# Kernel optimization log

Hardware: AMD Instinct MI355X
Metric: run time of the kernel (lower is better)

Reference implementation:

```python
import jax, jax.numpy as jnp
import numpy as np

N = 100000   # nodes
E = 1600000  # edges
IN = 128     # in_dim
H = 64       # hidden_dim
EPS = 1e-5


def layer_norm(x, g, b):
    mu = x.mean(-1, keepdims=True)
    v = ((x - mu) ** 2).mean(-1, keepdims=True)
    return (x - mu) * jax.lax.rsqrt(v + EPS) * g + b


def gcn_conv(x, W, b, src, dst, dinv):
    # PyG GCNConv: x' = D^{-1/2}(A+I)D^{-1/2} X W + b (degrees include self-loops)
    h = x @ W                                   # [N, H]
    coef = dinv[src] * dinv[dst]                # [E]
    agg = jax.ops.segment_sum(h[src] * coef[:, None], dst, num_segments=N)
    agg = agg + h * (dinv * dinv)[:, None]      # self-loop term
    return agg + b


def setup_inputs() -> dict:
    key = jax.random.key(0)
    ks = jax.random.split(key, 12)
    inp = {
        "x": jax.random.normal(ks[0], (N, IN), jnp.float32),
        "edge_index": jax.random.randint(ks[1], (2, E), 0, N, dtype=jnp.int64
                                         if jax.config.jax_enable_x64 else jnp.int32),
    }
    dims = [(IN, H), (H, H), (H, H)]
    for i, (di, do) in enumerate(dims, start=1):
        inp[f"W{i}"] = jax.random.normal(ks[2 * i], (di, do), jnp.float32) / np.sqrt(di)
        inp[f"b{i}"] = jnp.zeros((do,), jnp.float32)
        inp[f"g{i}"] = jnp.ones((do,), jnp.float32)
        inp[f"be{i}"] = jnp.zeros((do,), jnp.float32)
    inp["Wh"] = jax.random.normal(ks[11], (H, 1), jnp.float32) / np.sqrt(H)
    inp["bh"] = jnp.zeros((1,), jnp.float32)
    return inp


def reference(x, edge_index, W1, b1, g1, be1, W2, b2, g2, be2, W3, b3, g3, be3, Wh, bh):
    src, dst = edge_index[0], edge_index[1]
    deg = jax.ops.segment_sum(jnp.ones((E,), x.dtype), dst, num_segments=N) + 1.0
    dinv = jax.lax.rsqrt(deg)
    for W, b, g, be in ((W1, b1, g1, be1), (W2, b2, g2, be2), (W3, b3, g3, be3)):
        x = gcn_conv(x, W, b, src, dst, dinv)
        x = layer_norm(x, g, be)
        x = jax.nn.gelu(x, approximate=False)  # F.gelu default = exact erf
        # dropout omitted (eval mode / deterministic reference)
    return (x @ Wh + bh).squeeze(-1)  # [N]
```

## Files before the change

kernel.cpp:

```cpp
#include <hip/hip_runtime.h>
#include <math.h>

#define NODES 100000
#define EDGES 1600000
#define NBUCK 196
#define BCAP2 12288
#define EPB 4096

typedef __attribute__((ext_vector_type(8))) short short8;
typedef __attribute__((ext_vector_type(4))) float floatx4;
typedef __attribute__((ext_vector_type(4))) unsigned uv4;

__device__ __forceinline__ float gsum8(float x) {
#pragma unroll
  for (int o = 4; o > 0; o >>= 1) x += __shfl_xor(x, o, 64);
  return x;
}

__device__ __forceinline__ short f2bf(float f) {
  union { float f; unsigned u; } v;
  v.f = f;
  unsigned r = 0x7fffu + ((v.u >> 16) & 1u);
  return (short)((v.u + r) >> 16);
}
__device__ __forceinline__ float bflo(unsigned p) {
  union { unsigned u; float f; } v; v.u = p << 16; return v.f;
}
__device__ __forceinline__ float bfhi(unsigned p) {
  union { unsigned u; float f; } v; v.u = p & 0xffff0000u; return v.f;
}

__global__ __launch_bounds__(256) void k_bin2(const int* __restrict__ src,
                                              const int* __restrict__ dst,
                                              int* __restrict__ bins,
                                              int* __restrict__ gcur) {
  __shared__ int cnt[NBUCK], gbase[NBUCK], lcur[NBUCK];
  int t = threadIdx.x;
  for (int i = t; i < NBUCK; i += 256) cnt[i] = 0;
  __syncthreads();
  int base = blockIdx.x * EPB;
  int s[16], d[16];
#pragma unroll
  for (int j = 0; j < 16; ++j) {
    int e = base + j * 256 + t;
    if (e < EDGES) {
      s[j] = src[e];
      d[j] = dst[e];
      atomicAdd(&cnt[d[j] >> 9], 1);
    } else {
      d[j] = -1;
    }
  }
  __syncthreads();
  for (int i = t; i < NBUCK; i += 256) {
    int c = cnt[i];
    gbase[i] = c ? atomicAdd(&gcur[i], c) : 0;
    lcur[i] = 0;
  }
  __syncthreads();
#pragma unroll
  for (int j = 0; j < 16; ++j) {
    if (d[j] >= 0) {
      int bk = d[j] >> 9;
      int lp = atomicAdd(&lcur[bk], 1);
      int pos = gbase[bk] + lp;
      if (pos < BCAP2) bins[bk * BCAP2 + pos] = s[j] | ((d[j] & 511) << 17);
    }
  }
}

__global__ __launch_bounds__(256) void k_fillb2(const int* __restrict__ bins,
                                                const int* __restrict__ gcur,
                                                int* __restrict__ rowptr,
                                                float* __restrict__ dinv,
                                                int* __restrict__ csr) {
  __shared__ int bsm[256];
  __shared__ int cnt[512], cur[512], wtot[4];
  int b = blockIdx.x, t = threadIdx.x;
  int v = 0;
  if (t < NBUCK) { v = gcur[t]; if (v > BCAP2) v = BCAP2; }
  bsm[t] = v;
  cnt[t] = 0; cnt[t + 256] = 0;
  __syncthreads();
  for (int o = 1; o < 256; o <<= 1) {
    int u = (t >= o) ? bsm[t - o] : 0;
    __syncthreads();
    bsm[t] += u;
    __syncthreads();
  }
  if (b == 0 && t == NBUCK - 1) rowptr[NODES] = bsm[t];
  int cb = gcur[b]; if (cb > BCAP2) cb = BCAP2;
  int base = bsm[b] - cb;
  const int* bp = &bins[(size_t)b * BCAP2];
  for (int i = t; i < cb; i += 256)
    atomicAdd(&cnt[(bp[i] >> 17) & 511], 1);
  __syncthreads();
  int a0 = cnt[2 * t], a1 = cnt[2 * t + 1];
  int s = a0 + a1;
  int lane = t & 63, w = t >> 6;
  int inc = s;
#pragma unroll
  for (int o = 1; o < 64; o <<= 1) {
    int u = __shfl_up(inc, o, 64);
    if (lane >= o) inc += u;
  }
  if (lane == 63) wtot[w] = inc;
  __syncthreads();
  int wpre = 0;
  for (int ww = 0; ww < w; ++ww) wpre += wtot[ww];
  int r0 = base + wpre + inc - s;
  int r1 = r0 + a0;
  int n0 = b * 512 + 2 * t, n1 = n0 + 1;
  if (n0 < NODES) { rowptr[n0] = r0; dinv[n0] = rsqrtf((float)a0 + 1.0f); }
  if (n1 < NODES) { rowptr[n1] = r1; dinv[n1] = rsqrtf((float)a1 + 1.0f); }
  cur[2 * t] = r0; cur[2 * t + 1] = r1;
  __syncthreads();
  for (int i = t; i < cb; i += 256) {
    int pk = bp[i];
    int p = atomicAdd(&cur[(pk >> 17) & 511], 1);
    csr[p] = pk & 0x1FFFF;
  }
}

template <int K>
__global__ __launch_bounds__(256) void k_gemm_f32(const float* __restrict__ x,
                                                  const float* __restrict__ W,
                                                  const float* __restrict__ dinv,
                                                  short* __restrict__ hs) {
  constexpr int KP = K + 8;
  __shared__ __align__(16) short wt[64 * KP];
  for (int idx = threadIdx.x; idx < K * 64; idx += 256) {
    int k = idx >> 6, n = idx & 63;
    wt[n * KP + k] = f2bf(W[idx]);
  }
  __syncthreads();
  int wid = threadIdx.x >> 6, lane = threadIdx.x & 63;
  int tile = blockIdx.x * 4 + wid;
  if (tile * 16 >= NODES) return;
  int m = lane & 15, q = lane >> 4;

  short8 bfr[4][K / 32];
#pragma unroll
  for (int ct = 0; ct < 4; ++ct)
#pragma unroll
    for (int ks = 0; ks < K / 32; ++ks)
      bfr[ct][ks] = *reinterpret_cast<const short8*>(&wt[(ct * 16 + m) * KP + ks * 32 + q * 8]);

  floatx4 acc[4];
#pragma unroll
  for (int ct = 0; ct < 4; ++ct) acc[ct] = {0.f, 0.f, 0.f, 0.f};
  int r0 = tile * 16;
#pragma unroll
  for (int ks = 0; ks < K / 32; ++ks) {
    const float* xp = &x[(size_t)(r0 + m) * K + ks * 32 + q * 8];
    floatx4 a0 = *reinterpret_cast<const floatx4*>(xp);
    floatx4 a1 = *reinterpret_cast<const floatx4*>(xp + 4);
    short8 af;
#pragma unroll
    for (int j = 0; j < 4; ++j) { af[j] = f2bf(a0[j]); af[4 + j] = f2bf(a1[j]); }
#pragma unroll
    for (int ct = 0; ct < 4; ++ct)
      acc[ct] = __builtin_amdgcn_mfma_f32_16x16x32_bf16(af, bfr[ct][ks], acc[ct], 0, 0, 0);
  }
  float dv[4];
#pragma unroll
  for (int r = 0; r < 4; ++r) dv[r] = dinv[r0 + q * 4 + r];
#pragma unroll
  for (int ct = 0; ct < 4; ++ct)
#pragma unroll
    for (int r = 0; r < 4; ++r) {
      int row = r0 + q * 4 + r, col = ct * 16 + m;
      hs[row * 64 + col] = f2bf(acc[ct][r] * dv[r]);
    }
}

__global__ __launch_bounds__(256) void k_aggg(const short* __restrict__ hs,
                                              const float* __restrict__ dinv,
                                              const int* __restrict__ rowptr,
                                              const int* __restrict__ csr,
                                              const float* __restrict__ bias,
                                              const float* __restrict__ gam,
                                              const float* __restrict__ bet,
                                              const float* __restrict__ W,
                                              short* __restrict__ hsn) {
  __shared__ __align__(16) short wt[64 * 72];
  __shared__ __align__(16) short ut[32 * 72];
  int t = threadIdx.x;
  for (int idx = t; idx < 4096; idx += 256) {
    int k = idx >> 6, n = idx & 63;
    wt[n * 72 + k] = f2bf(W[idx]);
  }
  const uv4* hsv = (const uv4*)hs;
  int lane = t & 63, wid = t >> 6;
  int g = lane >> 3, q = lane & 7;
  int nb0 = blockIdx.x * 32;
  int r = wid * 8 + g;
  int n = nb0 + r;
  int e0 = rowptr[n], e1 = rowptr[n + 1];
  float dn = dinv[n];
  uv4 sv = hsv[(size_t)n * 8 + q];
  float acc[8];
#pragma unroll
  for (int w = 0; w < 4; ++w) { acc[2 * w] = bflo(sv[w]); acc[2 * w + 1] = bfhi(sv[w]); }

  int srcb = lane & 0x38;
  for (int base = e0; base < e1; base += 8) {
    int cnt = e1 - base;
    if (cnt > 8) cnt = 8;
    int a = base + (q < cnt ? q : 0);
    int sidx = csr[a];
    int s[8];
#pragma unroll
    for (int j = 0; j < 8; ++j) s[j] = __shfl(sidx, srcb | j, 64);
    uv4 v[8];
#pragma unroll
    for (int j = 0; j < 8; ++j) v[j] = hsv[(size_t)s[j] * 8 + q];
    if (cnt == 8) {
#pragma unroll
      for (int j = 0; j < 8; ++j)
#pragma unroll
        for (int w = 0; w < 4; ++w) { acc[2 * w] += bflo(v[j][w]); acc[2 * w + 1] += bfhi(v[j][w]); }
    } else {
#pragma unroll
      for (int j = 0; j < 8; ++j)
        if (j < cnt)
#pragma unroll
          for (int w = 0; w < 4; ++w) { acc[2 * w] += bflo(v[j][w]); acc[2 * w + 1] += bfhi(v[j][w]); }
    }
  }

  const floatx4* bi4 = (const floatx4*)bias;
  floatx4 b0 = bi4[q * 2], b1 = bi4[q * 2 + 1];
#pragma unroll
  for (int f = 0; f < 4; ++f) { acc[f] = acc[f] * dn + b0[f]; acc[f + 4] = acc[f + 4] * dn + b1[f]; }

  float lsum = 0.f;
#pragma unroll
  for (int f = 0; f < 8; ++f) lsum += acc[f];
  float mu = gsum8(lsum) * (1.0f / 64.0f);
  float d[8], lvar = 0.f;
#pragma unroll
  for (int f = 0; f < 8; ++f) { d[f] = acc[f] - mu; lvar += d[f] * d[f]; }
  float rs = rsqrtf(gsum8(lvar) * (1.0f / 64.0f) + 1e-5f);
  const floatx4* gm4 = (const floatx4*)gam;
  const floatx4* bt4 = (const floatx4*)bet;
  floatx4 g0 = gm4[q * 2], g1 = gm4[q * 2 + 1];
  floatx4 t0 = bt4[q * 2], t1 = bt4[q * 2 + 1];
  short8 us;
#pragma unroll
  for (int f = 0; f < 8; ++f) {
    float gv = (f < 4) ? g0[f] : g1[f - 4];
    float tv = (f < 4) ? t0[f] : t1[f - 4];
    float vv = d[f] * rs * gv + tv;
    float u = 0.5f * vv * (1.0f + erff(vv * 0.70710678118654752f));
    us[f] = f2bf(u * dn);
  }
  *reinterpret_cast<short8*>(&ut[r * 72 + q * 8]) = us;
  __syncthreads();

  int m = lane & 15, q2 = lane >> 4;
  int tile = wid >> 1, cb = (wid & 1) * 2;
  short8 bfr[2][2];
#pragma unroll
  for (int ct = 0; ct < 2; ++ct)
#pragma unroll
    for (int ks = 0; ks < 2; ++ks)
      bfr[ct][ks] = *reinterpret_cast<const short8*>(&wt[((cb + ct) * 16 + m) * 72 + ks * 32 + q2 * 8]);
  floatx4 ac[2];
#pragma unroll
  for (int ct = 0; ct < 2; ++ct) ac[ct] = {0.f, 0.f, 0.f, 0.f};
#pragma unroll
  for (int ks = 0; ks < 2; ++ks) {
    short8 af = *reinterpret_cast<const short8*>(&ut[(tile * 16 + m) * 72 + ks * 32 + q2 * 8]);
#pragma unroll
    for (int ct = 0; ct < 2; ++ct)
      ac[ct] = __builtin_amdgcn_mfma_f32_16x16x32_bf16(af, bfr[ct][ks], ac[ct], 0, 0, 0);
  }
#pragma unroll
  for (int ct = 0; ct < 2; ++ct)
#pragma unroll
    for (int rr = 0; rr < 4; ++rr) {
      int row = nb0 + tile * 16 + q2 * 4 + rr, col = (cb + ct) * 16 + m;
      hsn[row * 64 + col] = f2bf(ac[ct][rr]);
    }
}

__global__ __launch_bounds__(256) void k_agg_fin(const short* __restrict__ hs,
                                                 const float* __restrict__ dinv,
                                                 const int* __restrict__ rowptr,
                                                 const int* __restrict__ csr,
                                                 const float* __restrict__ bias,
                                                 const float* __restrict__ gam,
                                                 const float* __restrict__ bet,
                                                 const float* __restrict__ Wh,
                                                 const float* __restrict__ bh,
                                                 float* __restrict__ out) {
  const uv4* hsv = (const uv4*)hs;
  int lane = threadIdx.x & 63, wid = threadIdx.x >> 6;
  int g = lane >> 3, q = lane & 7;
  int n = blockIdx.x * 32 + wid * 8 + g;
  int e0 = rowptr[n], e1 = rowptr[n + 1];
  float dn = dinv[n];
  uv4 sv = hsv[(size_t)n * 8 + q];
  float acc[8];
#pragma unroll
  for (int w = 0; w < 4; ++w) { acc[2 * w] = bflo(sv[w]); acc[2 * w + 1] = bfhi(sv[w]); }
  int srcb = lane & 0x38;
  for (int base = e0; base < e1; base += 8) {
    int cnt = e1 - base;
    if (cnt > 8) cnt = 8;
    int a = base + (q < cnt ? q : 0);
    int sidx = csr[a];
    int s[8];
#pragma unroll
    for (int j = 0; j < 8; ++j) s[j] = __shfl(sidx, srcb | j, 64);
    uv4 v[8];
#pragma unroll
    for (int j = 0; j < 8; ++j) v[j] = hsv[(size_t)s[j] * 8 + q];
    if (cnt == 8) {
#pragma unroll
      for (int j = 0; j < 8; ++j)
#pragma unroll
        for (int w = 0; w < 4; ++w) { acc[2 * w] += bflo(v[j][w]); acc[2 * w + 1] += bfhi(v[j][w]); }
    } else {
#pragma unroll
      for (int j = 0; j < 8; ++j)
        if (j < cnt)
#pragma unroll
          for (int w = 0; w < 4; ++w) { acc[2 * w] += bflo(v[j][w]); acc[2 * w + 1] += bfhi(v[j][w]); }
    }
  }
  const floatx4* bi4 = (const floatx4*)bias;
  floatx4 b0 = bi4[q * 2], b1 = bi4[q * 2 + 1];
#pragma unroll
  for (int f = 0; f < 4; ++f) { acc[f] = acc[f] * dn + b0[f]; acc[f + 4] = acc[f + 4] * dn + b1[f]; }
  float lsum = 0.f;
#pragma unroll
  for (int f = 0; f < 8; ++f) lsum += acc[f];
  float mu = gsum8(lsum) * (1.0f / 64.0f);
  float d[8], lvar = 0.f;
#pragma unroll
  for (int f = 0; f < 8; ++f) { d[f] = acc[f] - mu; lvar += d[f] * d[f]; }
  float rs = rsqrtf(gsum8(lvar) * (1.0f / 64.0f) + 1e-5f);
  const floatx4* gm4 = (const floatx4*)gam;
  const floatx4* bt4 = (const floatx4*)bet;
  floatx4 g0 = gm4[q * 2], g1 = gm4[q * 2 + 1];
  floatx4 t0 = bt4[q * 2], t1 = bt4[q * 2 + 1];
  const floatx4* wh4 = (const floatx4*)Wh;
  floatx4 w0 = wh4[q * 2], w1 = wh4[q * 2 + 1];
  float lp = 0.f;
#pragma unroll
  for (int f = 0; f < 8; ++f) {
    float gv = (f < 4) ? g0[f] : g1[f - 4];
    float tv = (f < 4) ? t0[f] : t1[f - 4];
    float wv = (f < 4) ? w0[f] : w1[f - 4];
    float vv = d[f] * rs * gv + tv;
    float u = 0.5f * vv * (1.0f + erff(vv * 0.70710678118654752f));
    lp += u * wv;
  }
  float p = gsum8(lp);
  if (q == 0) out[n] = p + bh[0];
}

extern "C" void kernel_launch(void* const* d_in, const int* in_sizes, int n_in,
                              void* d_out, int out_size, void* d_ws, size_t ws_size,
                              hipStream_t stream) {
  const float* x  = (const float*)d_in[0];
  const int* ei   = (const int*)d_in[1];
  const float* W1 = (const float*)d_in[2];
  const float* b1 = (const float*)d_in[3];
  const float* g1 = (const float*)d_in[4];
  const float* be1= (const float*)d_in[5];
  const float* W2 = (const float*)d_in[6];
  const float* b2 = (const float*)d_in[7];
  const float* g2 = (const float*)d_in[8];
  const float* be2= (const float*)d_in[9];
  const float* W3 = (const float*)d_in[10];
  const float* b3 = (const float*)d_in[11];
  const float* g3 = (const float*)d_in[12];
  const float* be3= (const float*)d_in[13];
  const float* Wh = (const float*)d_in[14];
  const float* bh = (const float*)d_in[15];
  const int* srcp = ei;
  const int* dstp = ei + EDGES;

  char* ws = (char*)d_ws;
  size_t off = 0;
  auto take = [&](size_t bytes) {
    char* p = ws + off;
    off = (off + bytes + 255) & ~(size_t)255;
    return p;
  };
  float* dinv = (float*)take((size_t)NODES * 4);
  int* rowptr = (int*)take((size_t)(NODES + 1) * 4);
  int* csr    = (int*)take((size_t)EDGES * 4);
  short* hs_a = (short*)take((size_t)NODES * 64 * 2);
  short* hs_b = (short*)take((size_t)NODES * 64 * 2);
  int* bins   = (int*)hs_a;
  int* gcur   = (int*)hs_b;

  (void)hipMemsetAsync(gcur, 0, (size_t)NBUCK * 4, stream);
  k_bin2<<<(EDGES + EPB - 1) / EPB, 256, 0, stream>>>(srcp, dstp, bins, gcur);
  k_fillb2<<<NBUCK, 256, 0, stream>>>(bins, gcur, rowptr, dinv, csr);

  int gemm_grid = (NODES / 16 + 3) / 4;
  k_gemm_f32<128><<<gemm_grid, 256, 0, stream>>>(x, W1, dinv, hs_a);
  k_aggg<<<NODES / 32, 256, 0, stream>>>(hs_a, dinv, rowptr, csr, b1, g1, be1, W2, hs_b);
  k_aggg<<<NODES / 32, 256, 0, stream>>>(hs_b, dinv, rowptr, csr, b2, g2, be2, W3, hs_a);
  k_agg_fin<<<NODES / 32, 256, 0, stream>>>(hs_a, dinv, rowptr, csr, b3, g3, be3, Wh, bh, (float*)d_out);
}
```

Baseline: 277.7 us.

## Co-schedule edge binning with layer-1 GEMM and pre-convert weights

```diff
diff --git a/kernel.cpp b/kernel.cpp
--- a/kernel.cpp
+++ b/kernel.cpp
@@ -6,6 +6,9 @@
 #define NBUCK 196
 #define BCAP2 12288
 #define EPB 4096
+#define BINB 391
+#define GEMMB 1563
+#define G1 782
 
 typedef __attribute__((ext_vector_type(8))) short short8;
 typedef __attribute__((ext_vector_type(4))) float floatx4;
@@ -30,15 +33,16 @@
   union { unsigned u; float f; } v; v.u = p & 0xffff0000u; return v.f;
 }
 
-__global__ __launch_bounds__(256) void k_bin2(const int* __restrict__ src,
-                                              const int* __restrict__ dst,
-                                              int* __restrict__ bins,
-                                              int* __restrict__ gcur) {
-  __shared__ int cnt[NBUCK], gbase[NBUCK], lcur[NBUCK];
+__device__ __forceinline__ void bin_body(char* smemraw, int b, const int* __restrict__ src,
+                                         const int* __restrict__ dst, int* __restrict__ bins,
+                                         int* __restrict__ gcur) {
+  int* cnt = (int*)smemraw;
+  int* gbase = cnt + NBUCK;
+  int* lcur = gbase + NBUCK;
   int t = threadIdx.x;
   for (int i = t; i < NBUCK; i += 256) cnt[i] = 0;
   __syncthreads();
-  int base = blockIdx.x * EPB;
+  int base = b * EPB;
   int s[16], d[16];
 #pragma unroll
   for (int j = 0; j < 16; ++j) {
@@ -69,14 +73,14 @@
   }
 }
 
-__global__ __launch_bounds__(256) void k_fillb2(const int* __restrict__ bins,
-                                                const int* __restrict__ gcur,
-                                                int* __restrict__ rowptr,
-                                                float* __restrict__ dinv,
-                                                int* __restrict__ csr) {
-  __shared__ int bsm[256];
-  __shared__ int cnt[512], cur[512], wtot[4];
-  int b = blockIdx.x, t = threadIdx.x;
+__device__ __forceinline__ void fill_body(char* smemraw, int b, const int* __restrict__ bins,
+                                          const int* __restrict__ gcur, int* __restrict__ rowptr,
+                                          float* __restrict__ dinv, int* __restrict__ csr) {
+  int* bsm = (int*)smemraw;
+  int* cnt = bsm + 256;
+  int* cur = cnt + 512;
+  int* wtot = cur + 512;
+  int t = threadIdx.x;
   int v = 0;
   if (t < NBUCK) { v = gcur[t]; if (v > BCAP2) v = BCAP2; }
   bsm[t] = v;
@@ -96,9 +100,9 @@
     atomicAdd(&cnt[(bp[i] >> 17) & 511], 1);
   __syncthreads();
   int a0 = cnt[2 * t], a1 = cnt[2 * t + 1];
-  int s = a0 + a1;
+  int sum2 = a0 + a1;
   int lane = t & 63, w = t >> 6;
-  int inc = s;
+  int inc = sum2;
 #pragma unroll
   for (int o = 1; o < 64; o <<= 1) {
     int u = __shfl_up(inc, o, 64);
@@ -108,7 +112,7 @@
   __syncthreads();
   int wpre = 0;
   for (int ww = 0; ww < w; ++ww) wpre += wtot[ww];
-  int r0 = base + wpre + inc - s;
+  int r0 = base + wpre + inc - sum2;
   int r1 = r0 + a0;
   int n0 = b * 512 + 2 * t, n1 = n0 + 1;
   if (n0 < NODES) { rowptr[n0] = r0; dinv[n0] = rsqrtf((float)a0 + 1.0f); }
@@ -122,20 +126,17 @@
   }
 }
 
-template <int K>
-__global__ __launch_bounds__(256) void k_gemm_f32(const float* __restrict__ x,
-                                                  const float* __restrict__ W,
-                                                  const float* __restrict__ dinv,
-                                                  short* __restrict__ hs) {
-  constexpr int KP = K + 8;
-  __shared__ __align__(16) short wt[64 * KP];
+__device__ __forceinline__ void gemm_body(char* smemraw, int tile0, const float* __restrict__ x,
+                                          const float* __restrict__ W, short* __restrict__ hs) {
+  constexpr int K = 128, KP = K + 8;
+  short* wt = (short*)smemraw;
   for (int idx = threadIdx.x; idx < K * 64; idx += 256) {
     int k = idx >> 6, n = idx & 63;
     wt[n * KP + k] = f2bf(W[idx]);
   }
   __syncthreads();
   int wid = threadIdx.x >> 6, lane = threadIdx.x & 63;
-  int tile = blockIdx.x * 4 + wid;
+  int tile = tile0 + wid;
   if (tile * 16 >= NODES) return;
   int m = lane & 15, q = lane >> 4;
 
@@ -162,18 +163,126 @@
     for (int ct = 0; ct < 4; ++ct)
       acc[ct] = __builtin_amdgcn_mfma_f32_16x16x32_bf16(af, bfr[ct][ks], acc[ct], 0, 0, 0);
   }
-  float dv[4];
-#pragma unroll
-  for (int r = 0; r < 4; ++r) dv[r] = dinv[r0 + q * 4 + r];
 #pragma unroll
   for (int ct = 0; ct < 4; ++ct)
 #pragma unroll
     for (int r = 0; r < 4; ++r) {
       int row = r0 + q * 4 + r, col = ct * 16 + m;
-      hs[row * 64 + col] = f2bf(acc[ct][r] * dv[r]);
+      hs[row * 64 + col] = f2bf(acc[ct][r]);
     }
 }
 
+__device__ __forceinline__ void prepw_body(int p, const float* __restrict__ W2,
+                                           const float* __restrict__ W3,
+                                           short* __restrict__ wt2, short* __restrict__ wt3) {
+  const float* W = (p < 4) ? W2 : W3;
+  short* wt = (p < 4) ? wt2 : wt3;
+  int b0 = (p & 3) * 1024;
+  for (int i = threadIdx.x; i < 1024; i += 256) {
+    int e = b0 + i;
+    int k = e >> 6, n = e & 63;
+    wt[n * 72 + k] = f2bf(W[e]);
+  }
+}
+
+__device__ __forceinline__ void acc8(float acc[8], const uv4 (&v)[8], const float (&wj)[8]) {
+#pragma unroll
+  for (int j = 0; j < 8; ++j)
+#pragma unroll
+    for (int w = 0; w < 4; ++w) {
+      acc[2 * w]     += wj[j] * bflo(v[j][w]);
+      acc[2 * w + 1] += wj[j] * bfhi(v[j][w]);
+    }
+}
+
+template <bool PRESCALED>
+__device__ __forceinline__ void do_agg(const uv4* __restrict__ hsv, const float* __restrict__ dinv,
+                                       const int* __restrict__ csr, int n, int e0, int e1,
+                                       int lane, float dn, float acc[8]) {
+  int q = lane & 7, srcb = lane & 0x38;
+  uv4 sv = hsv[(size_t)n * 8 + q];
+#pragma unroll
+  for (int w = 0; w < 4; ++w) {
+    float lo = bflo(sv[w]), hi = bfhi(sv[w]);
+    if constexpr (PRESCALED) { acc[2 * w] = lo; acc[2 * w + 1] = hi; }
+    else { acc[2 * w] = lo * dn; acc[2 * w + 1] = hi * dn; }
+  }
+  int deg = e1 - e0;
+  if (deg <= 0) return;
+  int p0 = e0 + q, p1 = p0 + 8, p2 = p0 + 16, p3 = p0 + 24;
+  int i0 = csr[p0 < e1 ? p0 : e0];
+  int i1 = csr[p1 < e1 ? p1 : e0];
+  int i2 = csr[p2 < e1 ? p2 : e0];
+  int i3 = csr[p3 < e1 ? p3 : e0];
+  float g0 = 1.0f, g1 = 1.0f, g2 = 1.0f, g3 = 1.0f;
+  if constexpr (!PRESCALED) { g0 = dinv[i0]; g1 = dinv[i1]; g2 = dinv[i2]; g3 = dinv[i3]; }
+  int cA = min(deg, 8);
+  int cB = min(max(deg - 8, 0), 8);
+  int cC = min(max(deg - 16, 0), 8);
+  int cD = min(max(deg - 24, 0), 8);
+  int sA[8], sB[8], sC[8], sD[8];
+#pragma unroll
+  for (int j = 0; j < 8; ++j) {
+    sA[j] = __shfl(i0, srcb | j, 64);
+    sB[j] = __shfl(i1, srcb | j, 64);
+  }
+  uv4 vA[8], vB[8];
+#pragma unroll
+  for (int j = 0; j < 8; ++j) vA[j] = hsv[(size_t)sA[j] * 8 + q];
+#pragma unroll
+  for (int j = 0; j < 8; ++j) vB[j] = hsv[(size_t)sB[j] * 8 + q];
+  float wA[8], wB[8], wC[8], wD[8];
+#pragma unroll
+  for (int j = 0; j < 8; ++j) {
+    float bA = 1.0f, bB = 1.0f;
+    if constexpr (!PRESCALED) { bA = __shfl(g0, srcb | j, 64); bB = __shfl(g1, srcb | j, 64); }
+    wA[j] = (j < cA) ? bA : 0.0f;
+    wB[j] = (j < cB) ? bB : 0.0f;
+  }
+#pragma unroll
+  for (int j = 0; j < 8; ++j) {
+    sC[j] = __shfl(i2, srcb | j, 64);
+    sD[j] = __shfl(i3, srcb | j, 64);
+    float bC = 1.0f, bD = 1.0f;
+    if constexpr (!PRESCALED) { bC = __shfl(g2, srcb | j, 64); bD = __shfl(g3, srcb | j, 64); }
+    wC[j] = (j < cC) ? bC : 0.0f;
+    wD[j] = (j < cD) ? bD : 0.0f;
+  }
+  acc8(acc, vA, wA);
+  uv4 vC[8];
+#pragma unroll
+  for (int j = 0; j < 8; ++j) vC[j] = hsv[(size_t)sC[j] * 8 + q];
+  acc8(acc, vB, wB);
+  uv4 vD[8];
+#pragma unroll
+  for (int j = 0; j < 8; ++j) vD[j] = hsv[(size_t)sD[j] * 8 + q];
+  acc8(acc, vC, wC);
+  acc8(acc, vD, wD);
+  if (deg > 32) {
+    for (int base = e0 + 32; base < e1; base += 8) {
+      int cnt = e1 - base;
+      if (cnt > 8) cnt = 8;
+      int a = base + (q < cnt ? q : 0);
+      int sidx = csr[a];
+      float gq = 1.0f;
+      if constexpr (!PRESCALED) gq = dinv[sidx];
+      int s[8]; float wj[8];
+#pragma unroll
+      for (int j = 0; j < 8; ++j) {
+        s[j] = __shfl(sidx, srcb | j, 64);
+        float bj = 1.0f;
+        if constexpr (!PRESCALED) bj = __shfl(gq, srcb | j, 64);
+        wj[j] = (j < cnt) ? bj : 0.0f;
+      }
+      uv4 v[8];
+#pragma unroll
+      for (int j = 0; j < 8; ++j) v[j] = hsv[(size_t)s[j] * 8 + q];
+      acc8(acc, v, wj);
+    }
+  }
+}
+
+template <bool PRESCALED>
 __global__ __launch_bounds__(256) void k_aggg(const short* __restrict__ hs,
                                               const float* __restrict__ dinv,
                                               const int* __restrict__ rowptr,
@@ -181,14 +290,15 @@
                                               const float* __restrict__ bias,
                                               const float* __restrict__ gam,
                                               const float* __restrict__ bet,
-                                              const float* __restrict__ W,
+                                              const short* __restrict__ wtg,
                                               short* __restrict__ hsn) {
   __shared__ __align__(16) short wt[64 * 72];
   __shared__ __align__(16) short ut[32 * 72];
   int t = threadIdx.x;
-  for (int idx = t; idx < 4096; idx += 256) {
-    int k = idx >> 6, n = idx & 63;
-    wt[n * 72 + k] = f2bf(W[idx]);
+  {
+    const int* wp = (const int*)wtg;
+    int* wd = (int*)wt;
+    for (int idx = t; idx < 2304; idx += 256) wd[idx] = wp[idx];
   }
   const uv4* hsv = (const uv4*)hs;
   int lane = t & 63, wid = t >> 6;
@@ -198,36 +308,8 @@
   int n = nb0 + r;
   int e0 = rowptr[n], e1 = rowptr[n + 1];
   float dn = dinv[n];
-  uv4 sv = hsv[(size_t)n * 8 + q];
   float acc[8];
-#pragma unroll
-  for (int w = 0; w < 4; ++w) { acc[2 * w] = bflo(sv[w]); acc[2 * w + 1] = bfhi(sv[w]); }
-
-  int srcb = lane & 0x38;
-  for (int base = e0; base < e1; base += 8) {
-    int cnt = e1 - base;
-    if (cnt > 8) cnt = 8;
-    int a = base + (q < cnt ? q : 0);
-    int sidx = csr[a];
-    int s[8];
-#pragma unroll
-    for (int j = 0; j < 8; ++j) s[j] = __shfl(sidx, srcb | j, 64);
-    uv4 v[8];
-#pragma unroll
-    for (int j = 0; j < 8; ++j) v[j] = hsv[(size_t)s[j] * 8 + q];
-    if (cnt == 8) {
-#pragma unroll
-      for (int j = 0; j < 8; ++j)
-#pragma unroll
-        for (int w = 0; w < 4; ++w) { acc[2 * w] += bflo(v[j][w]); acc[2 * w + 1] += bfhi(v[j][w]); }
-    } else {
-#pragma unroll
-      for (int j = 0; j < 8; ++j)
-        if (j < cnt)
-#pragma unroll
-          for (int w = 0; w < 4; ++w) { acc[2 * w] += bflo(v[j][w]); acc[2 * w + 1] += bfhi(v[j][w]); }
-    }
-  }
+  do_agg<PRESCALED>(hsv, dinv, csr, n, e0, e1, lane, dn, acc);
 
   const floatx4* bi4 = (const floatx4*)bias;
   floatx4 b0 = bi4[q * 2], b1 = bi4[q * 2 + 1];
@@ -301,35 +383,8 @@
   int n = blockIdx.x * 32 + wid * 8 + g;
   int e0 = rowptr[n], e1 = rowptr[n + 1];
   float dn = dinv[n];
-  uv4 sv = hsv[(size_t)n * 8 + q];
   float acc[8];
-#pragma unroll
-  for (int w = 0; w < 4; ++w) { acc[2 * w] = bflo(sv[w]); acc[2 * w + 1] = bfhi(sv[w]); }
-  int srcb = lane & 0x38;
-  for (int base = e0; base < e1; base += 8) {
-    int cnt = e1 - base;
-    if (cnt > 8) cnt = 8;
-    int a = base + (q < cnt ? q : 0);
-    int sidx = csr[a];
-    int s[8];
-#pragma unroll
-    for (int j = 0; j < 8; ++j) s[j] = __shfl(sidx, srcb | j, 64);
-    uv4 v[8];
-#pragma unroll
-    for (int j = 0; j < 8; ++j) v[j] = hsv[(size_t)s[j] * 8 + q];
-    if (cnt == 8) {
-#pragma unroll
-      for (int j = 0; j < 8; ++j)
-#pragma unroll
-        for (int w = 0; w < 4; ++w) { acc[2 * w] += bflo(v[j][w]); acc[2 * w + 1] += bfhi(v[j][w]); }
-    } else {
-#pragma unroll
-      for (int j = 0; j < 8; ++j)
-        if (j < cnt)
-#pragma unroll
-          for (int w = 0; w < 4; ++w) { acc[2 * w] += bflo(v[j][w]); acc[2 * w + 1] += bfhi(v[j][w]); }
-    }
-  }
+  do_agg<true>(hsv, dinv, csr, n, e0, e1, lane, dn, acc);
   const floatx4* bi4 = (const floatx4*)bias;
   floatx4 b0 = bi4[q * 2], b1 = bi4[q * 2 + 1];
 #pragma unroll
@@ -360,6 +415,47 @@
   }
   float p = gsum8(lp);
   if (q == 0) out[n] = p + bh[0];
+}
+
+__global__ __launch_bounds__(256) void k_pre1(const int* __restrict__ src, const int* __restrict__ dst,
+                                              int* __restrict__ bins, int* __restrict__ gcur,
+                                              const float* __restrict__ x, const float* __restrict__ W1,
+                                              short* __restrict__ hs,
+                                              const float* __restrict__ W2, const float* __restrict__ W3,
+                                              short* __restrict__ wt2, short* __restrict__ wt3) {
+  __shared__ __align__(16) char smem[64 * 136 * 2];
+  int b = blockIdx.x;
+  if (b < BINB) bin_body(smem, b, src, dst, bins, gcur);
+  else if (b < BINB + G1) gemm_body(smem, (b - BINB) * 4, x, W1, hs);
+  else prepw_body(b - BINB - G1, W2, W3, wt2, wt3);
+}
+
+__global__ __launch_bounds__(256) void k_pre2(const int* __restrict__ bins, const int* __restrict__ gcur,
+                                              int* __restrict__ rowptr, float* __restrict__ dinv,
+                                              int* __restrict__ csr,
+                                              const float* __restrict__ x, const float* __restrict__ W1,
+                                              short* __restrict__ hs) {
+  __shared__ __align__(16) char smem[64 * 136 * 2];
+  int b = blockIdx.x;
+  if (b < NBUCK) fill_body(smem, b, bins, gcur, rowptr, dinv, csr);
+  else gemm_body(smem, (G1 + (b - NBUCK)) * 4, x, W1, hs);
+}
+
+__global__ __launch_bounds__(256) void k_bin2(const int* src, const int* dst, int* bins, int* gcur) {
+  __shared__ __align__(16) char smem[64 * 136 * 2];
+  bin_body(smem, blockIdx.x, src, dst, bins, gcur);
+}
+__global__ __launch_bounds__(256) void k_fillb2(const int* bins, const int* gcur, int* rowptr,
+                                                float* dinv, int* csr) {
+  __shared__ __align__(16) char smem[64 * 136 * 2];
+  fill_body(smem, blockIdx.x, bins, gcur, rowptr, dinv, csr);
+}
+__global__ __launch_bounds__(256) void k_gemm(const float* x, const float* W, short* hs) {
+  __shared__ __align__(16) char smem[64 * 136 * 2];
+  gemm_body(smem, blockIdx.x * 4, x, W, hs);
+}
+__global__ __launch_bounds__(256) void k_prepw(const float* W2, const float* W3, short* wt2, short* wt3) {
+  prepw_body(blockIdx.x, W2, W3, wt2, wt3);
 }
 
 extern "C" void kernel_launch(void* const* d_in, const int* in_sizes, int n_in,
@@ -396,16 +492,31 @@
   int* csr    = (int*)take((size_t)EDGES * 4);
   short* hs_a = (short*)take((size_t)NODES * 64 * 2);
   short* hs_b = (short*)take((size_t)NODES * 64 * 2);
-  int* bins   = (int*)hs_a;
-  int* gcur   = (int*)hs_b;
+  short* wt2  = (short*)take((size_t)64 * 72 * 2);
+  short* wt3  = (short*)take((size_t)64 * 72 * 2);
+
+  size_t bins_sz = (size_t)NBUCK * BCAP2 * 4;
+  bool overlap = (ws_size >= off + bins_sz + 4096);
+  int* bins; int* gcur;
+  if (overlap) {
+    bins = (int*)take(bins_sz);
+    gcur = (int*)take((size_t)NBUCK * 4);
+  } else {
+    bins = (int*)hs_a;
+    gcur = (int*)hs_b;
+  }
 
   (void)hipMemsetAsync(gcur, 0, (size_t)NBUCK * 4, stream);
-  k_bin2<<<(EDGES + EPB - 1) / EPB, 256, 0, stream>>>(srcp, dstp, bins, gcur);
-  k_fillb2<<<NBUCK, 256, 0, stream>>>(bins, gcur, rowptr, dinv, csr);
-
-  int gemm_grid = (NODES / 16 + 3) / 4;
-  k_gemm_f32<128><<<gemm_grid, 256, 0, stream>>>(x, W1, dinv, hs_a);
-  k_aggg<<<NODES / 32, 256, 0, stream>>>(hs_a, dinv, rowptr, csr, b1, g1, be1, W2, hs_b);
-  k_aggg<<<NODES / 32, 256, 0, stream>>>(hs_b, dinv, rowptr, csr, b2, g2, be2, W3, hs_a);
+  if (overlap) {
+    k_pre1<<<BINB + G1 + 8, 256, 0, stream>>>(srcp, dstp, bins, gcur, x, W1, hs_a, W2, W3, wt2, wt3);
+    k_pre2<<<NBUCK + (GEMMB - G1), 256, 0, stream>>>(bins, gcur, rowptr, dinv, csr, x, W1, hs_a);
+  } else {
+    k_bin2<<<BINB, 256, 0, stream>>>(srcp, dstp, bins, gcur);
+    k_fillb2<<<NBUCK, 256, 0, stream>>>(bins, gcur, rowptr, dinv, csr);
+    k_gemm<<<GEMMB, 256, 0, stream>>>(x, W1, hs_a);
+    k_prepw<<<8, 256, 0, stream>>>(W2, W3, wt2, wt3);
+  }
+  k_aggg<false><<<NODES / 32, 256, 0, stream>>>(hs_a, dinv, rowptr, csr, b1, g1, be1, wt2, hs_b);
+  k_aggg<true><<<NODES / 32, 256, 0, stream>>>(hs_b, dinv, rowptr, csr, b2, g2, be2, wt3, hs_a);
   k_agg_fin<<<NODES / 32, 256, 0, stream>>>(hs_a, dinv, rowptr, csr, b3, g3, be3, Wh, bh, (float*)d_out);
 }
```

Measured after the change: 274.4 us. Within noise of the previous version (-1.2%).
